# Kernel optimization log

Measured on AMD Instinct MI355X. Metric: run time of the kernel, lower is better.

## Reference

```python
import jax, jax.numpy as jnp
import numpy as np

B, T, F = 64, 1024, 4
INF = jnp.float32(1e30)


def _dtw_cost(p, q):
    """Accumulated DTW cost matrix. p: [T1,2], q: [T2,2]. Returns C: [T1,T2].

    Recurrence C[i,j] = D[i,j] + min(C[i-1,j], C[i,j-1], C[i-1,j-1]).
    The within-row dependency c_j = d_j + min(a_j, c_{j-1}) (with
    a_j = min(C[i-1,j], C[i-1,j-1])) is a min-plus scan, solved in closed
    form: c_j = S_j + cummin_k<=j (a_k - S_{k-1}), S = cumsum(d).
    """
    # pairwise Euclidean distance (dtw.dtw2d uses 2D Euclidean)
    D = jnp.sqrt(jnp.sum((p[:, None, :] - q[None, :, :]) ** 2, axis=-1))  # [T1,T2]

    c0 = jnp.cumsum(D[0])  # first row: only left moves allowed

    def row(prev, d):
        shifted = jnp.concatenate([jnp.full((1,), INF, prev.dtype), prev[:-1]])
        a = jnp.minimum(prev, shifted)          # min(C[i-1,j], C[i-1,j-1])
        S = jnp.cumsum(d)
        Sprev = jnp.concatenate([jnp.zeros((1,), d.dtype), S[:-1]])
        m = jax.lax.associative_scan(jnp.minimum, a - Sprev)
        c = S + m
        return c, c

    _, rest = jax.lax.scan(row, c0, D[1:])
    return jnp.concatenate([c0[None, :], rest], axis=0)


def _dtw_path(C):
    """Backtrace alignment path from C. Returns (a, b, valid) each [T1+T2-1]."""
    T1, T2 = C.shape
    L = T1 + T2 - 1

    def step(carry, _):
        i, j, done = carry
        at0 = (i == 0) & (j == 0)
        cd = jnp.where((i > 0) & (j > 0), C[i - 1, j - 1], INF)
        cu = jnp.where(i > 0, C[i - 1, j], INF)
        cl = jnp.where(j > 0, C[i, j - 1], INF)
        k = jnp.argmin(jnp.stack([cd, cu, cl]))  # diag preferred on ties
        di = jnp.where(k == 2, 0, 1)
        dj = jnp.where(k == 1, 0, 1)
        ni = jnp.where(at0, 0, i - di)
        nj = jnp.where(at0, 0, j - dj)
        return (ni, nj, done | at0), (i, j, jnp.logical_not(done))

    init = (jnp.int32(T1 - 1), jnp.int32(T2 - 1), jnp.bool_(False))
    _, (a, b, valid) = jax.lax.scan(step, init, None, length=L)
    return a, b, valid


def _single_loss(pred, targ, subcoef):
    # DTW alignment computed on (x, y) basis, detached (torch runs it in numpy)
    p = jax.lax.stop_gradient(pred[:, :2])
    q = jax.lax.stop_gradient(targ[:, :2])
    C = _dtw_cost(p, q)
    a, b, valid = _dtw_path(C)
    # gather aligned points on loss_indices = [0, 1], L1 loss weighted by subcoef
    pg = pred[a, :2]  # [L, 2]
    tg = targ[b, :2]
    w = valid[:, None].astype(pred.dtype)
    return jnp.sum(jnp.abs(pg - tg) * subcoef[None, :] * w)


def setup_inputs() -> dict:
    key = jax.random.key(0)
    k1, k2 = jax.random.split(key)
    preds = jax.random.normal(k1, (B, T, F), dtype=jnp.float32)
    targs = jax.random.normal(k2, (B, T, F), dtype=jnp.float32)
    subcoef = jnp.ones((2,), dtype=jnp.float32)
    return {"preds": preds, "targs": targs, "subcoef": subcoef}


def reference(preds, targs, subcoef):
    losses = jax.vmap(lambda p, t: _single_loss(p, t, subcoef))(preds, targs)
    return jnp.sum(losses)
```

## Files before the change

### kernel.cpp

```cpp
#include <hip/hip_runtime.h>

#define TT   1024
#define NW   34
#define FINF 1e30f

template<bool A> struct BoolC { static constexpr bool value = A; };


__global__ __launch_bounds__(512) void dtw_forward(
    const float* __restrict__ preds,
    const float* __restrict__ targs,
    uint2* __restrict__ dirs)
{
    __shared__ float2 qsh[TT];
    __shared__ float mbox[7][TT];

    const int tid  = threadIdx.x;
    const int w    = tid >> 6;
    const int lane = tid & 63;
    const int b    = blockIdx.x;

    for (int k = tid; k < TT; k += 512) {
        float4 t4 = ((const float4*)targs)[(size_t)b * TT + k];
        qsh[k] = make_float2(t4.x, t4.y);
    }
    for (int k = tid; k < 7 * TT; k += 512) ((float*)mbox)[k] = -1.0f;

    float pxA, pyA, pxB, pyB;
    {
        const int rowA = w * 128 + 2 * lane;
        float4 pv = ((const float4*)preds)[(size_t)b * TT + rowA];
        pxA = pv.x; pyA = pv.y;
        float4 pw = ((const float4*)preds)[(size_t)b * TT + rowA + 1];
        pxB = pw.x; pyB = pw.y;
    }
    __syncthreads();

    const float* src = (w > 0) ? mbox[w - 1] : nullptr;
    float*       dst = (w < 7) ? mbox[w]     : nullptr;

    float curA = FINF, curB = FINF, uprev = FINF, shp = FINF;
    unsigned auA = 0, adA = 0, auB = 0, adB = 0;
    float bnd[8];
#pragma unroll
    for (int k = 0; k < 8; ++k) bnd[k] = FINF;

    const int bi  = 2 * w + (lane >> 5);
    const int rr0 = 2 * (lane & 31);
    const bool is63 = (lane == 63);

    for (int T = 0; T < NW; ++T) {
        auto body = [&](auto actc) {
            constexpr bool ACT = decltype(actc)::value;
#pragma unroll 1
            for (int sub = 0; sub < 4; ++sub) {
                const int s0 = 32 * T + 8 * sub;
                float qx[8], qy[8];
#pragma unroll
                for (int k2 = 0; k2 < 8; ++k2) {
                    float2 qv = qsh[(s0 + k2 - lane) & (TT - 1)];
                    qx[k2] = qv.x; qy[k2] = qv.y;
                }
                if (w > 0 && s0 < TT) {
                    for (;;) {
                        unsigned sg = 0u;
#pragma unroll
                        for (int k2 = 0; k2 < 8; ++k2) {
                            bnd[k2] = __hip_atomic_load(src + s0 + k2, __ATOMIC_RELAXED,
                                                        __HIP_MEMORY_SCOPE_WORKGROUP);
                            sg |= __float_as_uint(bnd[k2]);
                        }
                        if (!(sg & 0x80000000u)) break;
                        __builtin_amdgcn_s_sleep(1);
                    }
                }
#pragma unroll
                for (int k2 = 0; k2 < 8; ++k2) {
                    const int s = s0 + k2;
                    const float dA = __builtin_amdgcn_sqrtf(
                        (pxA - qx[k2]) * (pxA - qx[k2]) + (pyA - qy[k2]) * (pyA - qy[k2]));
                    const float dB = __builtin_amdgcn_sqrtf(
                        (pxB - qx[k2]) * (pxB - qx[k2]) + (pyB - qy[k2]) * (pyB - qy[k2]));

                    const float u = (lane == 0) ? ((w == 0) ? FINF : bnd[k2]) : shp;
                    const float cAo = curA, cBo = curB;

                    float m2a = fminf(u, cAo);
                    float ba  = fminf(uprev, m2a);
                    if constexpr (ACT) ba = (ba > 9e29f) ? 0.0f : ba;
                    float vA = dA + ba;
                    unsigned bdA = (uprev <= m2a) ? 1u : 0u;
                    unsigned buA = ((u <= cAo) ? 1u : 0u) | bdA;
                    float m2b = fminf(vA, cBo);
                    float vB = dB + fminf(cAo, m2b);
                    unsigned bdB = (cAo <= m2b) ? 1u : 0u;
                    unsigned buB = ((vA <= cBo) ? 1u : 0u) | bdB;

                    auA = (auA << 1) | buA;  adA = (adA << 1) | bdA;
                    auB = (auB << 1) | buB;  adB = (adB << 1) | bdB;

                    if constexpr (ACT) {
                        const bool act = (lane <= s);
                        curA = act ? vA : cAo;
                        curB = act ? vB : cBo;
                    } else {
                        curA = vA; curB = vB;
                    }
                    uprev = u;

                    if (is63 && w < 7 && (unsigned)(s - 63) < 1024u)
                        __hip_atomic_store(dst + (s - 63), curB, __ATOMIC_RELAXED,
                                           __HIP_MEMORY_SCOPE_WORKGROUP);

                    shp = __shfl_up(curB, 1);
                }
            }
        };
        if (T < 2) body(BoolC<true>{}); else body(BoolC<false>{});
        dirs[(size_t)((b * 16 + bi) * NW + T) * 64 + rr0] =
            make_uint2(__builtin_bitreverse32(auA), __builtin_bitreverse32(adA));
        dirs[(size_t)((b * 16 + bi) * NW + T) * 64 + rr0 + 1] =
            make_uint2(__builtin_bitreverse32(auB), __builtin_bitreverse32(adB));
        auA = adA = auB = adB = 0u;
    }
}

__global__ __launch_bounds__(1024) void dtw_exits(
    const uint2* __restrict__ dirs,
    unsigned short* __restrict__ exitc)
{
    __shared__ uint2 raw[NW * 64];
    __shared__ unsigned nebit[64][32];
    __shared__ unsigned dgbit[64][32];

    const int tid = threadIdx.x;
    const int b = blockIdx.x >> 4, bi = blockIdx.x & 15;

    for (int i = tid; i < NW * 64; i += 1024)
        raw[i] = dirs[(size_t)(b * 16 + bi) * (NW * 64) + i];
    __syncthreads();
    for (int i = tid; i < 64 * 32; i += 1024) {
        const int rr = i >> 5, u = i & 31;
        const int o  = ((bi & 1) << 5) + (rr >> 1);
        const int T0 = u + (o >> 5), sh = o & 31;
        uint2 A  = raw[T0 * 64 + rr];
        uint2 Bv = raw[(T0 + 1) * 64 + rr];
        nebit[rr][u] = sh ? ((A.x >> sh) | (Bv.x << (32 - sh))) : A.x;
        dgbit[rr][u] = sh ? ((A.y >> sh) | (Bv.y << (32 - sh))) : A.y;
    }
    __syncthreads();

    int j = tid;
    for (int rr = 63; rr >= 0; --rr) {
        if (bi == 0 && rr == 0) { j = 0; break; }
        int u = j >> 5, m = j & 31;
        unsigned wv = nebit[rr][u] << (31 - m);
        while (wv == 0u) { --u; wv = nebit[rr][u]; m = 31; }
        const int j2 = (u << 5) + m - __builtin_clz(wv);
        const int diag = (int)((dgbit[rr][j2 >> 5] >> (j2 & 31)) & 1u);
        j = j2 - diag;
    }
    exitc[((size_t)(b * 16 + bi) << 10) + tid] = (unsigned short)j;
}

__global__ void dtw_entries(const unsigned short* __restrict__ exitc,
                            unsigned short* __restrict__ ent)
{
    const int b = threadIdx.x;
    int j = TT - 1;
    for (int bi = 15; bi >= 0; --bi) {
        ent[b * 16 + bi] = (unsigned short)j;
        j = exitc[((size_t)(b * 16 + bi) << 10) + j];
    }
}

__global__ __launch_bounds__(64) void dtw_loss(
    const float* __restrict__ preds,
    const float* __restrict__ targs,
    const float* __restrict__ subcoef,
    const uint2* __restrict__ dirs,
    const unsigned short* __restrict__ ent,
    float* __restrict__ out)
{
    __shared__ uint2 raw[NW * 64];
    __shared__ unsigned nebit[64][32];
    __shared__ unsigned dgbit[64][32];
    __shared__ float2 qsh[TT];
    __shared__ float2 psh[64];
    __shared__ unsigned recs[160];

    const int lane = threadIdx.x;
    const int b = blockIdx.x >> 4, bi = blockIdx.x & 15;

    for (int i = lane; i < NW * 64; i += 64)
        raw[i] = dirs[(size_t)(b * 16 + bi) * (NW * 64) + i];
    for (int k = lane; k < TT; k += 64) {
        float4 t4 = ((const float4*)targs)[(size_t)b * TT + k];
        qsh[k] = make_float2(t4.x, t4.y);
    }
    {
        float4 p4 = ((const float4*)preds)[(size_t)b * TT + bi * 64 + lane];
        psh[lane] = make_float2(p4.x, p4.y);
    }
    __syncthreads();
    for (int i = lane; i < 64 * 32; i += 64) {
        const int rr = i >> 5, u = i & 31;
        const int o  = ((bi & 1) << 5) + (rr >> 1);
        const int T0 = u + (o >> 5), sh = o & 31;
        uint2 A  = raw[T0 * 64 + rr];
        uint2 Bv = raw[(T0 + 1) * 64 + rr];
        nebit[rr][u] = sh ? ((A.x >> sh) | (Bv.x << (32 - sh))) : A.x;
        dgbit[rr][u] = sh ? ((A.y >> sh) | (Bv.y << (32 - sh))) : A.y;
    }
    __syncthreads();

    int j = ent[b * 16 + bi];
    int nrec = 0;
    for (int rr = 63; rr >= 0; --rr) {
        int j2;
        if (bi == 0 && rr == 0) j2 = 0;
        else {
            int u = j >> 5, m = j & 31;
            unsigned wv = nebit[rr][u] << (31 - m);
            while (wv == 0u) { --u; wv = nebit[rr][u]; m = 31; }
            j2 = (u << 5) + m - __builtin_clz(wv);
        }
        int c = j;
        for (;;) {
            int cl = (c - 31 > j2) ? (c - 31) : j2;
            if (lane == 0)
                recs[nrec] = ((unsigned)rr << 20) | ((unsigned)cl << 10) | (unsigned)c;
            ++nrec;
            if (cl == j2) break;
            c = cl - 1;
        }
        if (bi == 0 && rr == 0) j = 0;
        else {
            const int diag = (int)((dgbit[rr][j2 >> 5] >> (j2 & 31)) & 1u);
            j = j2 - diag;
        }
    }
    __syncthreads();

    const float sc0 = subcoef[0], sc1 = subcoef[1];
    float acc = 0.0f;
    for (int k = lane; k < nrec; k += 64) {
        unsigned rec = recs[k];
        int rr = (int)(rec >> 20), cl = (int)((rec >> 10) & 1023u), ch = (int)(rec & 1023u);
        float2 p = psh[rr];
        for (int c = cl; c <= ch; ++c) {
            float2 q = qsh[c];
            acc += fabsf(p.x - q.x) * sc0 + fabsf(p.y - q.y) * sc1;
        }
    }
    for (int o = 32; o; o >>= 1) acc += __shfl_down(acc, o);
    if (lane == 0) atomicAdd(out, acc);
}

extern "C" void kernel_launch(void* const* d_in, const int* in_sizes, int n_in,
                              void* d_out, int out_size, void* d_ws, size_t ws_size,
                              hipStream_t stream)
{
    const float* preds   = (const float*)d_in[0];
    const float* targs   = (const float*)d_in[1];
    const float* subcoef = (const float*)d_in[2];
    float* out = (float*)d_out;

    const int B = in_sizes[0] / (TT * 4);

    const size_t dirsBytes = (size_t)B * 16 * NW * 64 * sizeof(uint2);
    const size_t exitBytes = (size_t)B * 16 * 1024 * sizeof(unsigned short);
    uint2* dirs = (uint2*)d_ws;
    unsigned short* exitc = (unsigned short*)((char*)d_ws + dirsBytes);
    unsigned short* ent   = (unsigned short*)((char*)d_ws + dirsBytes + exitBytes);

    hipMemsetAsync(out, 0, sizeof(float), stream);
    dtw_forward<<<dim3(B), dim3(512), 0, stream>>>(preds, targs, dirs);
    dtw_exits<<<dim3(B * 16), dim3(1024), 0, stream>>>(dirs, exitc);
    dtw_entries<<<dim3(1), dim3(B), 0, stream>>>(exitc, ent);
    dtw_loss<<<dim3(B * 16), dim3(64), 0, stream>>>(preds, targs, subcoef, dirs, ent, out);
}
```

Baseline: 420.8 us.

## Use 4 rows per lane and barrier-phased wavefront instead of spin-wait mailboxes

The forward DTW kernel now has each lane own 4 rows with 4 waves per block, where it previously used 2 rows per lane and 8 waves. The atomic spin-wait mailbox handoff between waves is replaced by a global phase loop with __syncthreads, where each wave lags the one above it by 3 tiles. The lane shift uses a DPP row shift, and direction bits are written as uint4 stores. The downstream bit-extraction offsets change to match the new layout, and the backtrace gains bounds guards. The cost is a longer per-lane serial chain, fewer waves per block, and extra pipeline fill phases, in exchange for removing spin polling and shuffle overhead.

After: 411.9 us. 1.02x faster.

```diff
diff --git a/kernel.cpp b/kernel.cpp
--- a/kernel.cpp
+++ b/kernel.cpp
@@ -2,126 +2,152 @@
 
 #define TT   1024
 #define NW   34
+#define NPH  (NW + 9)
 #define FINF 1e30f
 
 template<bool A> struct BoolC { static constexpr bool value = A; };
 
 
-__global__ __launch_bounds__(512) void dtw_forward(
+__device__ __forceinline__ float dpp_wave_shr1(float x) {
+    return __int_as_float(__builtin_amdgcn_update_dpp(
+        0, __float_as_int(x), 0x138, 0xF, 0xF, false));
+}
+
+__global__ __launch_bounds__(256) void dtw_forward(
     const float* __restrict__ preds,
     const float* __restrict__ targs,
     uint2* __restrict__ dirs)
 {
     __shared__ float2 qsh[TT];
-    __shared__ float mbox[7][TT];
+    __shared__ float  mbox[3][TT];
 
     const int tid  = threadIdx.x;
     const int w    = tid >> 6;
     const int lane = tid & 63;
     const int b    = blockIdx.x;
 
-    for (int k = tid; k < TT; k += 512) {
+    for (int k = tid; k < TT; k += 256) {
         float4 t4 = ((const float4*)targs)[(size_t)b * TT + k];
         qsh[k] = make_float2(t4.x, t4.y);
     }
-    for (int k = tid; k < 7 * TT; k += 512) ((float*)mbox)[k] = -1.0f;
-
-    float pxA, pyA, pxB, pyB;
+    for (int k = tid; k < 3 * TT; k += 256) ((float*)mbox)[k] = FINF;
+
+    float px[4], py[4];
     {
-        const int rowA = w * 128 + 2 * lane;
-        float4 pv = ((const float4*)preds)[(size_t)b * TT + rowA];
-        pxA = pv.x; pyA = pv.y;
-        float4 pw = ((const float4*)preds)[(size_t)b * TT + rowA + 1];
-        pxB = pw.x; pyB = pw.y;
+        const int row0 = w * 256 + 4 * lane;
+#pragma unroll
+        for (int r = 0; r < 4; ++r) {
+            float4 pv = ((const float4*)preds)[(size_t)b * TT + row0 + r];
+            px[r] = pv.x; py[r] = pv.y;
+        }
     }
     __syncthreads();
 
     const float* src = (w > 0) ? mbox[w - 1] : nullptr;
-    float*       dst = (w < 7) ? mbox[w]     : nullptr;
-
-    float curA = FINF, curB = FINF, uprev = FINF, shp = FINF;
-    unsigned auA = 0, adA = 0, auB = 0, adB = 0;
+    float*       dst = (w < 3) ? mbox[w]     : nullptr;
+
+    float cur0 = FINF, cur1 = FINF, cur2 = FINF, cur3 = FINF;
+    float uprev = FINF, shp = FINF;
+    unsigned au0 = 0, ad0 = 0, au1 = 0, ad1 = 0;
+    unsigned au2 = 0, ad2 = 0, au3 = 0, ad3 = 0;
     float bnd[8];
 #pragma unroll
     for (int k = 0; k < 8; ++k) bnd[k] = FINF;
 
-    const int bi  = 2 * w + (lane >> 5);
-    const int rr0 = 2 * (lane & 31);
+    const int bi  = 4 * w + (lane >> 4);
+    const int rr0 = 4 * (lane & 15);
     const bool is63 = (lane == 63);
 
-    for (int T = 0; T < NW; ++T) {
-        auto body = [&](auto actc) {
-            constexpr bool ACT = decltype(actc)::value;
+    for (int G = 0; G < NPH; ++G) {
+        const int T = G - 3 * w;
+        if ((unsigned)T < (unsigned)NW) {
+            auto body = [&](auto actc) {
+                constexpr bool ACT = decltype(actc)::value;
 #pragma unroll 1
-            for (int sub = 0; sub < 4; ++sub) {
-                const int s0 = 32 * T + 8 * sub;
-                float qx[8], qy[8];
-#pragma unroll
-                for (int k2 = 0; k2 < 8; ++k2) {
-                    float2 qv = qsh[(s0 + k2 - lane) & (TT - 1)];
-                    qx[k2] = qv.x; qy[k2] = qv.y;
-                }
-                if (w > 0 && s0 < TT) {
-                    for (;;) {
-                        unsigned sg = 0u;
+                for (int sub = 0; sub < 4; ++sub) {
+                    const int s0 = 32 * T + 8 * sub;
+                    float qx[8], qy[8];
+#pragma unroll
+                    for (int k2 = 0; k2 < 8; ++k2) {
+                        float2 qv = qsh[(s0 + k2 - lane) & (TT - 1)];
+                        qx[k2] = qv.x; qy[k2] = qv.y;
+                    }
+                    if (w > 0 && s0 < TT) {
+#pragma unroll
+                        for (int k2 = 0; k2 < 8; ++k2) bnd[k2] = src[s0 + k2];
+                    }
+                    float bq[8];
+#pragma unroll
+                    for (int k2 = 0; k2 < 8; ++k2) {
+                        const int s = s0 + k2;
+                        float d[4];
+#pragma unroll
+                        for (int r = 0; r < 4; ++r) {
+                            const float dx = px[r] - qx[k2];
+                            const float dy = py[r] - qy[k2];
+                            d[r] = __builtin_amdgcn_sqrtf(dx * dx + dy * dy);
+                        }
+
+                        const float u = (lane == 0) ? ((w == 0) ? FINF : bnd[k2]) : shp;
+                        const float c0o = cur0, c1o = cur1, c2o = cur2, c3o = cur3;
+
+                        float m2a = fminf(u, c0o);
+                        float ba  = fminf(uprev, m2a);
+                        if constexpr (ACT) ba = (ba > 9e29f) ? 0.0f : ba;
+                        const float v0 = d[0] + ba;
+                        const unsigned bd0 = (uprev <= m2a) ? 1u : 0u;
+                        const unsigned bu0 = ((u <= c0o) ? 1u : 0u) | bd0;
+                        float m2b = fminf(v0, c1o);
+                        const float v1 = d[1] + fminf(c0o, m2b);
+                        const unsigned bd1 = (c0o <= m2b) ? 1u : 0u;
+                        const unsigned bu1 = ((v0 <= c1o) ? 1u : 0u) | bd1;
+                        float m2c = fminf(v1, c2o);
+                        const float v2 = d[2] + fminf(c1o, m2c);
+                        const unsigned bd2 = (c1o <= m2c) ? 1u : 0u;
+                        const unsigned bu2 = ((v1 <= c2o) ? 1u : 0u) | bd2;
+                        float m2d = fminf(v2, c3o);
+                        const float v3 = d[3] + fminf(c2o, m2d);
+                        const unsigned bd3 = (c2o <= m2d) ? 1u : 0u;
+                        const unsigned bu3 = ((v2 <= c3o) ? 1u : 0u) | bd3;
+
+                        au0 = (au0 << 1) | bu0;  ad0 = (ad0 << 1) | bd0;
+                        au1 = (au1 << 1) | bu1;  ad1 = (ad1 << 1) | bd1;
+                        au2 = (au2 << 1) | bu2;  ad2 = (ad2 << 1) | bd2;
+                        au3 = (au3 << 1) | bu3;  ad3 = (ad3 << 1) | bd3;
+
+                        if constexpr (ACT) {
+                            const bool act = (lane <= s);
+                            cur0 = act ? v0 : c0o;
+                            cur1 = act ? v1 : c1o;
+                            cur2 = act ? v2 : c2o;
+                            cur3 = act ? v3 : c3o;
+                        } else {
+                            cur0 = v0; cur1 = v1; cur2 = v2; cur3 = v3;
+                        }
+                        uprev = u;
+                        bq[k2] = cur3;
+                        shp = dpp_wave_shr1(cur3);
+                    }
+                    if (is63 && w < 3) {
 #pragma unroll
                         for (int k2 = 0; k2 < 8; ++k2) {
-                            bnd[k2] = __hip_atomic_load(src + s0 + k2, __ATOMIC_RELAXED,
-                                                        __HIP_MEMORY_SCOPE_WORKGROUP);
-                            sg |= __float_as_uint(bnd[k2]);
+                            const int c = s0 + k2 - 63;
+                            if ((unsigned)c < 1024u) dst[c] = bq[k2];
                         }
-                        if (!(sg & 0x80000000u)) break;
-                        __builtin_amdgcn_s_sleep(1);
                     }
                 }
-#pragma unroll
-                for (int k2 = 0; k2 < 8; ++k2) {
-                    const int s = s0 + k2;
-                    const float dA = __builtin_amdgcn_sqrtf(
-                        (pxA - qx[k2]) * (pxA - qx[k2]) + (pyA - qy[k2]) * (pyA - qy[k2]));
-                    const float dB = __builtin_amdgcn_sqrtf(
-                        (pxB - qx[k2]) * (pxB - qx[k2]) + (pyB - qy[k2]) * (pyB - qy[k2]));
-
-                    const float u = (lane == 0) ? ((w == 0) ? FINF : bnd[k2]) : shp;
-                    const float cAo = curA, cBo = curB;
-
-                    float m2a = fminf(u, cAo);
-                    float ba  = fminf(uprev, m2a);
-                    if constexpr (ACT) ba = (ba > 9e29f) ? 0.0f : ba;
-                    float vA = dA + ba;
-                    unsigned bdA = (uprev <= m2a) ? 1u : 0u;
-                    unsigned buA = ((u <= cAo) ? 1u : 0u) | bdA;
-                    float m2b = fminf(vA, cBo);
-                    float vB = dB + fminf(cAo, m2b);
-                    unsigned bdB = (cAo <= m2b) ? 1u : 0u;
-                    unsigned buB = ((vA <= cBo) ? 1u : 0u) | bdB;
-
-                    auA = (auA << 1) | buA;  adA = (adA << 1) | bdA;
-                    auB = (auB << 1) | buB;  adB = (adB << 1) | bdB;
-
-                    if constexpr (ACT) {
-                        const bool act = (lane <= s);
-                        curA = act ? vA : cAo;
-                        curB = act ? vB : cBo;
-                    } else {
-                        curA = vA; curB = vB;
-                    }
-                    uprev = u;
-
-                    if (is63 && w < 7 && (unsigned)(s - 63) < 1024u)
-                        __hip_atomic_store(dst + (s - 63), curB, __ATOMIC_RELAXED,
-                                           __HIP_MEMORY_SCOPE_WORKGROUP);
-
-                    shp = __shfl_up(curB, 1);
-                }
-            }
-        };
-        if (T < 2) body(BoolC<true>{}); else body(BoolC<false>{});
-        dirs[(size_t)((b * 16 + bi) * NW + T) * 64 + rr0] =
-            make_uint2(__builtin_bitreverse32(auA), __builtin_bitreverse32(adA));
-        dirs[(size_t)((b * 16 + bi) * NW + T) * 64 + rr0 + 1] =
-            make_uint2(__builtin_bitreverse32(auB), __builtin_bitreverse32(adB));
-        auA = adA = auB = adB = 0u;
+            };
+            if (T < 2) body(BoolC<true>{}); else body(BoolC<false>{});
+
+            const size_t base = (size_t)((b * 16 + bi) * NW + T) * 64 + rr0;
+            uint4* dp = (uint4*)&dirs[base];
+            dp[0] = make_uint4(__builtin_bitreverse32(au0), __builtin_bitreverse32(ad0),
+                               __builtin_bitreverse32(au1), __builtin_bitreverse32(ad1));
+            dp[1] = make_uint4(__builtin_bitreverse32(au2), __builtin_bitreverse32(ad2),
+                               __builtin_bitreverse32(au3), __builtin_bitreverse32(ad3));
+            au0 = ad0 = au1 = ad1 = au2 = ad2 = au3 = ad3 = 0u;
+        }
+        __syncthreads();
     }
 }
 
@@ -141,7 +167,7 @@
     __syncthreads();
     for (int i = tid; i < 64 * 32; i += 1024) {
         const int rr = i >> 5, u = i & 31;
-        const int o  = ((bi & 1) << 5) + (rr >> 1);
+        const int o  = ((bi & 3) << 4) + (rr >> 2);
         const int T0 = u + (o >> 5), sh = o & 31;
         uint2 A  = raw[T0 * 64 + rr];
         uint2 Bv = raw[(T0 + 1) * 64 + rr];
@@ -155,10 +181,11 @@
         if (bi == 0 && rr == 0) { j = 0; break; }
         int u = j >> 5, m = j & 31;
         unsigned wv = nebit[rr][u] << (31 - m);
-        while (wv == 0u) { --u; wv = nebit[rr][u]; m = 31; }
-        const int j2 = (u << 5) + m - __builtin_clz(wv);
+        while (wv == 0u && u > 0) { --u; wv = nebit[rr][u]; m = 31; }
+        const int j2 = (wv == 0u) ? 0 : ((u << 5) + m - __builtin_clz(wv));
         const int diag = (int)((dgbit[rr][j2 >> 5] >> (j2 & 31)) & 1u);
         j = j2 - diag;
+        if (j < 0) j = 0;
     }
     exitc[((size_t)(b * 16 + bi) << 10) + tid] = (unsigned short)j;
 }
@@ -205,7 +232,7 @@
     __syncthreads();
     for (int i = lane; i < 64 * 32; i += 64) {
         const int rr = i >> 5, u = i & 31;
-        const int o  = ((bi & 1) << 5) + (rr >> 1);
+        const int o  = ((bi & 3) << 4) + (rr >> 2);
         const int T0 = u + (o >> 5), sh = o & 31;
         uint2 A  = raw[T0 * 64 + rr];
         uint2 Bv = raw[(T0 + 1) * 64 + rr];
@@ -222,8 +249,8 @@
         else {
             int u = j >> 5, m = j & 31;
             unsigned wv = nebit[rr][u] << (31 - m);
-            while (wv == 0u) { --u; wv = nebit[rr][u]; m = 31; }
-            j2 = (u << 5) + m - __builtin_clz(wv);
+            while (wv == 0u && u > 0) { --u; wv = nebit[rr][u]; m = 31; }
+            j2 = (wv == 0u) ? 0 : ((u << 5) + m - __builtin_clz(wv));
         }
         int c = j;
         for (;;) {
@@ -238,6 +265,7 @@
         else {
             const int diag = (int)((dgbit[rr][j2 >> 5] >> (j2 & 31)) & 1u);
             j = j2 - diag;
+            if (j < 0) j = 0;
         }
     }
     __syncthreads();
@@ -275,7 +303,7 @@
     unsigned short* ent   = (unsigned short*)((char*)d_ws + dirsBytes + exitBytes);
 
     hipMemsetAsync(out, 0, sizeof(float), stream);
-    dtw_forward<<<dim3(B), dim3(512), 0, stream>>>(preds, targs, dirs);
+    dtw_forward<<<dim3(B), dim3(256), 0, stream>>>(preds, targs, dirs);
     dtw_exits<<<dim3(B * 16), dim3(1024), 0, stream>>>(dirs, exitc);
     dtw_entries<<<dim3(1), dim3(B), 0, stream>>>(exitc, ent);
     dtw_loss<<<dim3(B * 16), dim3(64), 0, stream>>>(preds, targs, subcoef, dirs, ent, out);
```
